# Kernel optimization log

Hardware: AMD Instinct MI355X
Metric: run time of the kernel (lower is better)

## Reference

```python
import jax, jax.numpy as jnp
import numpy as np

BN_EPS = 1e-5
N_SH, N_SS, N_HH, D = 1195, 390, 805, 64


def _gcn(x, edge_index, W, b, n_nodes, mean):
    # per-edge message = Linear(x_j); lin(x)[src] == lin(x[src])
    h = x @ W + b                                   # [N, out]
    msg = h[edge_index[0]]                          # gather sources -> [E, out]
    agg = jax.ops.segment_sum(msg, edge_index[1], num_segments=n_nodes)
    if mean:
        cnt = jax.ops.segment_sum(jnp.ones((edge_index.shape[1],), x.dtype),
                                  edge_index[1], num_segments=n_nodes)
        agg = agg / jnp.maximum(cnt, 1.0)[:, None]
    return jnp.tanh(agg)


def _bn(x, gamma, beta):
    # BatchNorm1d in training mode: biased batch statistics
    m = jnp.mean(x, axis=0)
    v = jnp.var(x, axis=0)
    return (x - m) * jax.lax.rsqrt(v + BN_EPS) * gamma + beta


def setup_inputs() -> dict:
    key = jax.random.key(0)
    ks = jax.random.split(key, 40)
    f32 = jnp.float32

    def lin(k, din, dout):
        k1, k2 = jax.random.split(k)
        s = 1.0 / np.sqrt(din)
        W = jax.random.uniform(k1, (din, dout), f32, -s, s)
        b = jax.random.uniform(k2, (dout,), f32, -s, s)
        return W, b

    inp = {}
    inp["x_SH"] = jnp.arange(N_SH, dtype=jnp.int64 if jax.config.jax_enable_x64 else jnp.int32)
    inp["edge_index_SH"] = jax.random.randint(ks[0], (2, 1_000_000), 0, N_SH)
    inp["x_SS"] = jnp.arange(N_SS)
    inp["edge_index_SS"] = jax.random.randint(ks[1], (2, 200_000), 0, N_SS)
    inp["x_HH"] = jnp.arange(N_HH)
    inp["edge_index_HH"] = jax.random.randint(ks[2], (2, 200_000), 0, N_HH)
    inp["prescription"] = jax.random.uniform(ks[3], (20000, N_SS), f32)
    inp["kgOneHot"] = jax.random.uniform(ks[4], (N_HH, 27), f32)

    inp["emb"] = jax.random.normal(ks[5], (N_SH, D), f32)
    inp["w_sh1"], inp["b_sh1"] = lin(ks[6], D, D)
    inp["w_sh2"], inp["b_sh2"] = lin(ks[7], D, D)
    inp["w_mlp1"], inp["b_mlp1"] = lin(ks[8], D, 256)
    inp["g_bn1"] = jnp.ones((256,), f32); inp["be_bn1"] = jnp.zeros((256,), f32)
    inp["w_sh1h"], inp["b_sh1h"] = lin(ks[9], D, D)
    inp["w_sh2h"], inp["b_sh2h"] = lin(ks[10], D, D)
    inp["w_mlp1h"], inp["b_mlp1h"] = lin(ks[11], D, 256)
    inp["g_bn1h"] = jnp.ones((256,), f32); inp["be_bn1h"] = jnp.zeros((256,), f32)
    inp["w_ss"], inp["b_ss"] = lin(ks[12], D, 256)
    inp["w_hh"], inp["b_hh"] = lin(ks[13], D + 27, 256)
    inp["w_mlp"], inp["b_mlp"] = lin(ks[14], 256, 256)
    inp["g_si"] = jnp.ones((256,), f32); inp["be_si"] = jnp.zeros((256,), f32)
    return inp


def reference(x_SH, edge_index_SH, x_SS, edge_index_SS, x_HH, edge_index_HH,
              prescription, kgOneHot, emb,
              w_sh1, b_sh1, w_sh2, b_sh2, w_mlp1, b_mlp1, g_bn1, be_bn1,
              w_sh1h, b_sh1h, w_sh2h, b_sh2h, w_mlp1h, b_mlp1h, g_bn1h, be_bn1h,
              w_ss, b_ss, w_hh, b_hh, w_mlp, b_mlp, g_si, be_si):
    # symptom branch on SH graph (mean aggregation)
    x1 = emb[x_SH]                                           # [1195, 64]
    x2 = _gcn(x1, edge_index_SH, w_sh1, b_sh1, N_SH, mean=True)
    x6 = _gcn(x2, edge_index_SH, w_sh2, b_sh2, N_SH, mean=True)
    x9 = (x1 + x2 + x6) / 3.0
    x9 = jnp.tanh(_bn(x9 @ w_mlp1 + b_mlp1, g_bn1, be_bn1))  # [1195, 256]

    # herb branch on SH graph
    x22 = _gcn(x1, edge_index_SH, w_sh1h, b_sh1h, N_SH, mean=True)
    x66 = _gcn(x22, edge_index_SH, w_sh2h, b_sh2h, N_SH, mean=True)
    x99 = (x1 + x22 + x66) / 3.0
    x99 = jnp.tanh(_bn(x99 @ w_mlp1h + b_mlp1h, g_bn1h, be_bn1h))

    # SS graph (add aggregation)
    x_ss1 = _gcn(emb[x_SS], edge_index_SS, w_ss, b_ss, N_SS, mean=False)  # [390, 256]

    # HH graph with KG one-hot features appended
    x_hh0 = jnp.concatenate([emb[x_HH], kgOneHot], axis=-1)  # [805, 91]
    x_hh1 = _gcn(x_hh0, edge_index_HH, w_hh, b_hh, N_HH, mean=False)      # [805, 256]

    es = x9[:N_SS] + x_ss1                                   # [390, 256]
    eh = x99[N_SS:] + x_hh1                                  # [805, 256]

    e_synd = prescription @ es                               # [B, 256]
    pre_sum = jnp.sum(prescription, axis=1, keepdims=True)
    e = e_synd / pre_sum
    e = jax.nn.relu(_bn(e @ w_mlp + b_mlp, g_si, be_si))
    return e @ eh.T                                          # [B, 805]
```

## Files before the change

### kernel.cpp

```cpp
#include <hip/hip_runtime.h>
#include <cstddef>
#include <cstdint>

#define N_SH 1195
#define N_SS 390
#define N_HH 805
#define DIM  64

typedef __bf16 bf16_t;
typedef bf16_t bf16x4v __attribute__((ext_vector_type(4)));
typedef bf16_t bf16x8v __attribute__((ext_vector_type(8)));
typedef float f32x4 __attribute__((ext_vector_type(4)));

__device__ inline ushort f2bf(float f) {
    union { float f; uint32_t u; } c; c.f = f;
    uint32_t u = c.u;
    u += 0x7FFFu + ((u >> 16) & 1u);
    return (ushort)(u >> 16);
}

__device__ inline void xcd_swizzle(int gx, int gy, int& bx, int& by) {
    int nwg = gx * gy;
    int lin = by * gx + bx;
    int q = nwg >> 3, r = nwg & 7;
    int xcd = lin & 7, idx = lin >> 3;
    int nt = (xcd < r ? xcd * (q + 1) : r * (q + 1) + (xcd - r) * q) + idx;
    by = nt / gx; bx = nt % gx;
}

__global__ void build_adj3_kernel(
    const int* __restrict__ e1, int E1, int hs1, uint32_t* __restrict__ T1,
    const int* __restrict__ e2, int E2, int hs2, uint32_t* __restrict__ T2,
    const int* __restrict__ e3, int E3, int hs3, uint32_t* __restrict__ T3)
{
    int i = blockIdx.x * blockDim.x + threadIdx.x;
    if (i < E1) {
        int src = e1[i], dst = e1[E1 + i];
        atomicAdd(&T1[(size_t)dst * hs1 + (src >> 2)], 1u << ((src & 3) * 8));
    } else if (i < E1 + E2) {
        int j = i - E1;
        int src = e2[j], dst = e2[E2 + j];
        atomicAdd(&T2[(size_t)dst * hs2 + (src >> 2)], 1u << ((src & 3) * 8));
    } else if (i < E1 + E2 + E3) {
        int j = i - E1 - E2;
        int src = e3[j], dst = e3[E3 + j];
        atomicAdd(&T3[(size_t)dst * hs3 + (src >> 2)], 1u << ((src & 3) * 8));
    }
}

__device__ inline void unpack_one(const uint32_t* __restrict__ T, int R, int C,
                                  int hs, ushort* __restrict__ out, int Cp, int i) {
    int r = i / Cp, c = i % Cp;
    float v = 0.f;
    if (r < R && c < C) {
        uint32_t w = T[(size_t)r * hs + (c >> 2)];
        v = (float)((w >> ((c & 3) * 8)) & 0xFFu);
    }
    out[i] = f2bf(v);
}

__global__ void mega_prep_kernel(
    const uint32_t* __restrict__ T1, int hs1, ushort* __restrict__ o1, int n1, int Cp1,
    const uint32_t* __restrict__ T2, int hs2, ushort* __restrict__ o2, int n2, int Cp2,
    const uint32_t* __restrict__ T3, int hs3, ushort* __restrict__ o3, int n3, int Cp3,
    float* __restrict__ cntInv,
    const float* __restrict__ w_sh1, const float* __restrict__ w_sh1h,
    const float* __restrict__ b_sh1, const float* __restrict__ b_sh1h,
    const float* __restrict__ w_sh2, const float* __restrict__ w_sh2h,
    const float* __restrict__ b_sh2, const float* __restrict__ b_sh2h,
    const float* __restrict__ w_mlp1, const float* __restrict__ w_mlp1h,
    const float* __restrict__ b_mlp1, const float* __restrict__ b_mlp1h,
    float* __restrict__ W1cat, float* __restrict__ b1cat,
    float* __restrict__ W2bd,  float* __restrict__ b2cat,
    float* __restrict__ WMbd,  float* __restrict__ bMcat,
    const float* __restrict__ emb, const float* __restrict__ kg,
    float* __restrict__ xhh0)
{
    int i = blockIdx.x * blockDim.x + threadIdx.x;
    if (i < n1) { unpack_one(T1, N_SH, N_SH, hs1, o1, Cp1, i); return; }
    i -= n1;
    if (i < n2) { unpack_one(T2, N_SS, N_SS, hs2, o2, Cp2, i); return; }
    i -= n2;
    if (i < n3) { unpack_one(T3, N_HH, N_HH, hs3, o3, Cp3, i); return; }
    i -= n3;
    if (i < N_SH * 64) {
        int row = i >> 6, lane = i & 63;
        const uint32_t* p = T1 + (size_t)row * hs1;
        uint32_t s = 0;
        for (int c = lane; c < hs1; c += 64) {
            uint32_t w0 = p[c];
            s += (w0 & 0xFFu) + ((w0 >> 8) & 0xFFu) + ((w0 >> 16) & 0xFFu) + (w0 >> 24);
        }
        for (int off = 32; off > 0; off >>= 1) s += __shfl_down(s, off);
        if (lane == 0) cntInv[row] = 1.0f / fmaxf((float)s, 1.0f);
        return;
    }
    i -= N_SH * 64;
    if (i < 64 * 128) {
        int k = i >> 7, j = i & 127;
        W1cat[i] = (j < 64) ? w_sh1[k * 64 + j] : w_sh1h[k * 64 + (j - 64)];
        return;
    }
    i -= 64 * 128;
    if (i < 128) { b1cat[i] = (i < 64) ? b_sh1[i] : b_sh1h[i - 64]; return; }
    i -= 128;
    if (i < 128 * 128) {
        int k = i >> 7, j = i & 127;
        float v = 0.f;
        if (k < 64 && j < 64) v = w_sh2[k * 64 + j];
        else if (k >= 64 && j >= 64) v = w_sh2h[(k - 64) * 64 + (j - 64)];
        W2bd[i] = v;
        return;
    }
    i -= 128 * 128;
    if (i < 128) { b2cat[i] = (i < 64) ? b_sh2[i] : b_sh2h[i - 64]; return; }
    i -= 128;
    if (i < 128 * 512) {
        int k = i >> 9, j = i & 511;
        float v = 0.f;
        if (j < 256) { if (k < 64) v = w_mlp1[k * 256 + j]; }
        else         { if (k >= 64) v = w_mlp1h[(k - 64) * 256 + (j - 256)]; }
        WMbd[i] = v;
        return;
    }
    i -= 128 * 512;
    if (i < 512) { bMcat[i] = (i < 256) ? b_mlp1[i] : b_mlp1h[i - 256]; return; }
    i -= 512;
    if (i < N_HH * 91) {
        int r = i / 91, c = i % 91;
        xhh0[i] = (c < DIM) ? emb[r * DIM + c] : kg[r * 27 + (c - DIM)];
    }
}

#define BM 64
#define BN 64
#define BK 16

__global__ __launch_bounds__(256) void gemm_kernel(
    const float* __restrict__ A, const float* __restrict__ A2, int ldaA, int ldaA2,
    const float* __restrict__ B,
    const float* __restrict__ bias,
    float* __restrict__ C, ushort* __restrict__ outT, int ldt,
    int M, int N, int K, float* __restrict__ statsOut, int statsStride,
    const float* __restrict__ bnStats, const float* __restrict__ bnG,
    const float* __restrict__ bnBe, int bnM)
{
    __shared__ float As[BK][BM + 4];
    __shared__ float Bs[BK][BN];
    __shared__ float cs[128];
    __shared__ float sA[256], tA[256];
    const int tid  = threadIdx.x;
    const int row0 = blockIdx.y * BM;
    const int col0 = blockIdx.x * BN;
    const int tr  = (tid >> 4) << 2;
    const int tc  = (tid & 15) << 2;
    const int lar = tid >> 2;
    const int lac = (tid & 3) << 2;
    const int lbr = tid >> 4;
    const int lbc = (tid & 15) << 2;

    if (bnStats) {
        float invM = 1.0f / (float)bnM;
        float mean = bnStats[tid] * invM;
        float var  = fmaxf(bnStats[512 + tid] * invM - mean * mean, 0.f);
        float scv  = bnG[tid] * rsqrtf(var + 1e-5f);
        sA[tid] = scv;
        tA[tid] = bnBe[tid] - mean * scv;
        __syncthreads();
    }

    float acc[4][4] = {{0.f}};

    for (int k0 = 0; k0 < K; k0 += BK) {
        const int gr = row0 + lar;
        #pragma unroll
        for (int i = 0; i < 4; ++i) {
            int gk = k0 + lac + i;
            float v = 0.f;
            if (gr < M && gk < K) {
                v = A[(size_t)gr * ldaA + gk];
                if (bnStats) v = tanhf(v * sA[gk] + tA[gk]);
                if (A2) v += A2[(size_t)gr * ldaA2 + gk];
            }
            As[lac + i][lar] = v;
        }
        const int gk = k0 + lbr;
        const float* Bp = B + (size_t)gk * N + col0 + lbc;
        #pragma unroll
        for (int i = 0; i < 4; ++i) {
            int gc = col0 + lbc + i;
            Bs[lbr][lbc + i] = (gk < K && gc < N) ? Bp[i] : 0.f;
        }
        __syncthreads();
        #pragma unroll
        for (int kk = 0; kk < BK; ++kk) {
            float4 a = *reinterpret_cast<const float4*>(&As[kk][tr]);
            float4 b = *reinterpret_cast<const float4*>(&Bs[kk][tc]);
            acc[0][0] += a.x * b.x; acc[0][1] += a.x * b.y; acc[0][2] += a.x * b.z; acc[0][3] += a.x * b.w;
            acc[1][0] += a.y * b.x; acc[1][1] += a.y * b.y; acc[1][2] += a.y * b.z; acc[1][3] += a.y * b.w;
            acc[2][0] += a.z * b.x; acc[2][1] += a.z * b.y; acc[2][2] += a.z * b.z; acc[2][3] += a.z * b.w;
            acc[3][0] += a.w * b.x; acc[3][1] += a.w * b.y; acc[3][2] += a.w * b.z; acc[3][3] += a.w * b.w;
        }
        __syncthreads();
    }

    float ls[4] = {0.f, 0.f, 0.f, 0.f}, lq[4] = {0.f, 0.f, 0.f, 0.f};
    #pragma unroll
    for (int i = 0; i < 4; ++i) {
        int gr = row0 + tr + i;
        if (gr >= M) continue;
        #pragma unroll
        for (int j = 0; j < 4; ++j) {
            int gc = col0 + tc + j;
            if (gc >= N) continue;
            float v = acc[i][j];
            if (bias) v += bias[gc];
            if (outT) outT[(size_t)gc * ldt + gr] = f2bf(v);
            else      C[(size_t)gr * N + gc] = v;
            ls[j] += v; lq[j] += v * v;
        }
    }

    if (statsOut) {
        if (tid < 128) cs[tid] = 0.f;
        __syncthreads();
        #pragma unroll
        for (int j = 0; j < 4; ++j) {
            atomicAdd(&cs[tc + j], ls[j]);
            atomicAdd(&cs[64 + tc + j], lq[j]);
        }
        __syncthreads();
        if (tid < 64) {
            atomicAdd(&statsOut[col0 + tid], cs[tid]);
            atomicAdd(&statsOut[statsStride + col0 + tid], cs[64 + tid]);
        }
    }
}

#define LDT 40
#define OLW 132

__device__ inline void loadP8(const float* __restrict__ rowp, int c0, bool rv,
                              float* a, float& s) {
    if (rv && c0 + 8 <= N_SS) {
        float2 x0 = *reinterpret_cast<const float2*>(rowp + c0);
        float2 x1 = *reinterpret_cast<const float2*>(rowp + c0 + 2);
        float2 x2 = *reinterpret_cast<const float2*>(rowp + c0 + 4);
        float2 x3 = *reinterpret_cast<const float2*>(rowp + c0 + 6);
        a[0] = x0.x; a[1] = x0.y; a[2] = x1.x; a[3] = x1.y;
        a[4] = x2.x; a[5] = x2.y; a[6] = x3.x; a[7] = x3.y;
    } else {
        #pragma unroll
        for (int i = 0; i < 8; ++i) a[i] = (rv && (c0 + i) < N_SS) ? rowp[c0 + i] : 0.f;
    }
    #pragma unroll
    for (int i = 0; i < 8; ++i) s += a[i];
}

__global__ __launch_bounds__(256) void mfma_c1_kernel(
    const float* __restrict__ Pm, const ushort* __restrict__ Dt,
    int M, const float* __restrict__ bias,
    float* __restrict__ outF, float* __restrict__ statsOut)
{
    __shared__ __align__(16) uint8_t smemRaw[128 * LDT * 2 * 2];
    ushort* As = (ushort*)smemRaw;
    ushort* Bs = (ushort*)(smemRaw + 128 * LDT * 2);
    float*  oLds = (float*)smemRaw;
    __shared__ float sums[128];
    __shared__ float cs[256];
    const int tid  = threadIdx.x;
    int bx = blockIdx.x, by = blockIdx.y;
    xcd_swizzle(gridDim.x, gridDim.y, bx, by);
    const int row0 = by * 128;
    const int col0 = bx * 128;
    const int wid  = tid >> 6, lane = tid & 63;
    const int wr = wid >> 1, wc = wid & 1;
    const int l15 = lane & 15, lg = lane >> 4;
    const int kg = lg * 4;
    const int sr = tid >> 2;
    const int sc = (tid & 3) * 8;

    const float* pA0 = Pm + (size_t)(row0 + sr)      * N_SS;
    const float* pA1 = Pm + (size_t)(row0 + sr + 64) * N_SS;
    const bool rv0 = (row0 + sr)      < M;
    const bool rv1 = (row0 + sr + 64) < M;
    const ushort* pB0 = Dt + (size_t)(col0 + sr)      * 416 + sc;
    const ushort* pB1 = Dt + (size_t)(col0 + sr + 64) * 416 + sc;

    float a0[8], a1[8];
    float s0 = 0.f, s1 = 0.f;
    loadP8(pA0, sc, rv0, a0, s0);
    loadP8(pA1, sc, rv1, a1, s1);
    uint4 b0 = *reinterpret_cast<const uint4*>(pB0);
    uint4 b1 = *reinterpret_cast<const uint4*>(pB1);

    f32x4 acc[4][4];
    #pragma unroll
    for (int m = 0; m < 4; ++m)
        #pragma unroll
        for (int n = 0; n < 4; ++n) acc[m][n] = (f32x4)0.f;

    for (int k0 = 0; k0 < 416; k0 += 32) {
        {
            bf16_t h[8];
            #pragma unroll
            for (int i = 0; i < 8; ++i) h[i] = (bf16_t)a0[i];
            *reinterpret_cast<uint4*>(&As[sr * LDT + sc]) = *reinterpret_cast<const uint4*>(h);
            #pragma unroll
            for (int i = 0; i < 8; ++i) h[i] = (bf16_t)a1[i];
            *reinterpret_cast<uint4*>(&As[(sr + 64) * LDT + sc]) = *reinterpret_cast<const uint4*>(h);
        }
        *reinterpret_cast<uint4*>(&Bs[sr * LDT + sc])        = b0;
        *reinterpret_cast<uint4*>(&Bs[(sr + 64) * LDT + sc]) = b1;
        __syncthreads();
        if (k0 + 32 < 416) {
            loadP8(pA0, k0 + 32 + sc, rv0, a0, s0);
            loadP8(pA1, k0 + 32 + sc, rv1, a1, s1);
            b0 = *reinterpret_cast<const uint4*>(pB0 + k0 + 32);
            b1 = *reinterpret_cast<const uint4*>(pB1 + k0 + 32);
        }

        bf16x8v af[4], bfr[4];
        #pragma unroll
        for (int m = 0; m < 4; ++m) {
            int ar = wr * 64 + m * 16 + l15;
            bf16x4v lo = *reinterpret_cast<const bf16x4v*>(&As[ar * LDT + kg]);
            bf16x4v hi = *reinterpret_cast<const bf16x4v*>(&As[ar * LDT + kg + 16]);
            af[m] = __builtin_shufflevector(lo, hi, 0, 1, 2, 3, 4, 5, 6, 7);
        }
        #pragma unroll
        for (int n = 0; n < 4; ++n) {
            int br = wc * 64 + n * 16 + l15;
            bf16x4v lo = *reinterpret_cast<const bf16x4v*>(&Bs[br * LDT + kg]);
            bf16x4v hi = *reinterpret_cast<const bf16x4v*>(&Bs[br * LDT + kg + 16]);
            bfr[n] = __builtin_shufflevector(lo, hi, 0, 1, 2, 3, 4, 5, 6, 7);
        }
        #pragma unroll
        for (int m = 0; m < 4; ++m)
            #pragma unroll
            for (int n = 0; n < 4; ++n)
                acc[m][n] = __builtin_amdgcn_mfma_f32_16x16x32_bf16(af[m], bfr[n], acc[m][n], 0, 0, 0);
        __syncthreads();
    }

    if (tid < 128) sums[tid] = 0.f;
    if (tid < 256) cs[tid] = 0.f;
    __syncthreads();
    atomicAdd(&sums[sr], s0);
    atomicAdd(&sums[sr + 64], s1);
    __syncthreads();

    float ls[4] = {0.f, 0.f, 0.f, 0.f}, lq[4] = {0.f, 0.f, 0.f, 0.f};
    #pragma unroll
    for (int m = 0; m < 4; ++m) {
        int lr_base = wr * 64 + m * 16 + kg;
        #pragma unroll
        for (int j = 0; j < 4; ++j) {
            int lr = lr_base + j;
            int grow = row0 + lr;
            float t = sums[lr];
            float inv = (t != 0.f) ? 1.0f / t : 0.f;
            #pragma unroll
            for (int n = 0; n < 4; ++n) {
                int gcol = col0 + wc * 64 + n * 16 + l15;
                float v = acc[m][n][j] * inv + bias[gcol];
                acc[m][n][j] = v;
                if (grow < M) { ls[n] += v; lq[n] += v * v; }
            }
        }
    }

    #pragma unroll
    for (int n = 0; n < 4; ++n) {
        int lc = wc * 64 + n * 16 + l15;
        atomicAdd(&cs[lc], ls[n]);
        atomicAdd(&cs[128 + lc], lq[n]);
    }
    __syncthreads();
    if (tid < 128) {
        atomicAdd(&statsOut[col0 + tid], cs[tid]);
        atomicAdd(&statsOut[256 + col0 + tid], cs[128 + tid]);
    }

    for (int m = 0; m < 4; ++m) {
        __syncthreads();
        #pragma unroll
        for (int n = 0; n < 4; ++n)
            #pragma unroll
            for (int j = 0; j < 4; ++j)
                oLds[(wr * 16 + kg + j) * OLW + wc * 64 + n * 16 + l15] = acc[m][n][j];
        __syncthreads();
        #pragma unroll
        for (int rr = 0; rr < 8; ++rr) {
            int lrow = wid * 8 + rr;
            int band = lrow >> 4;
            int r16  = lrow & 15;
            int grow = row0 + band * 64 + m * 16 + r16;
            if (grow < M) {
                float v0 = oLds[lrow * OLW + lane];
                float v1 = oLds[lrow * OLW + 64 + lane];
                outF[(size_t)grow * 256 + col0 + lane]      = v0;
                outF[(size_t)grow * 256 + col0 + 64 + lane] = v1;
            }
        }
    }
}

__global__ __launch_bounds__(256) void mfma_c3_kernel(
    const float* __restrict__ Abuf, const ushort* __restrict__ Bt,
    int M, int Nw,
    const float* __restrict__ stats, const float* __restrict__ g,
    const float* __restrict__ be,
    float* __restrict__ outF, int ldo)
{
    __shared__ __align__(16) uint8_t smemRaw[128 * LDT * 2 * 2];
    ushort* As = (ushort*)smemRaw;
    ushort* Bs = (ushort*)(smemRaw + 128 * LDT * 2);
    float*  oLds = (float*)smemRaw;
    __shared__ float sscale[256], sshift[256];
    const int tid  = threadIdx.x;
    int bx = blockIdx.x, by = blockIdx.y;
    xcd_swizzle(gridDim.x, gridDim.y, bx, by);
    const int row0 = by * 128;
    const int col0 = bx * 128;
    const int wid  = tid >> 6, lane = tid & 63;
    const int wr = wid >> 1, wc = wid & 1;
    const int l15 = lane & 15, lg = lane >> 4;
    const int kg = lg * 4;
    const int sr = tid >> 2;
    const int sc = (tid & 3) * 8;

    if (tid < 256) {
        float invM = 1.0f / (float)M;
        float mean = stats[tid] * invM;
        float var  = fmaxf(stats[256 + tid] * invM - mean * mean, 0.f);
        float scv  = g[tid] * rsqrtf(var + 1e-5f);
        sscale[tid] = scv;
        sshift[tid] = be[tid] - mean * scv;
    }
    __syncthreads();

    const float*  pA0 = Abuf + (size_t)(row0 + sr)      * 256 + sc;
    const float*  pA1 = Abuf + (size_t)(row0 + sr + 64) * 256 + sc;
    const ushort* pB0 = Bt + (size_t)(col0 + sr)        * 256 + sc;
    const ushort* pB1 = Bt + (size_t)(col0 + sr + 64)   * 256 + sc;

    float4 a00 = *reinterpret_cast<const float4*>(pA0);
    float4 a01 = *reinterpret_cast<const float4*>(pA0 + 4);
    float4 a10 = *reinterpret_cast<const float4*>(pA1);
    float4 a11 = *reinterpret_cast<const float4*>(pA1 + 4);
    uint4  b0  = *reinterpret_cast<const uint4*>(pB0);
    uint4  b1  = *reinterpret_cast<const uint4*>(pB1);

    f32x4 acc[4][4];
    #pragma unroll
    for (int m = 0; m < 4; ++m)
        #pragma unroll
        for (int n = 0; n < 4; ++n) acc[m][n] = (f32x4)0.f;

    for (int k0 = 0; k0 < 256; k0 += 32) {
        float s8[8], t8[8];
        #pragma unroll
        for (int i = 0; i < 8; ++i) { s8[i] = sscale[k0 + sc + i]; t8[i] = sshift[k0 + sc + i]; }
        {
            bf16_t h[8];
            h[0] = (bf16_t)fmaxf(a00.x * s8[0] + t8[0], 0.f);
            h[1] = (bf16_t)fmaxf(a00.y * s8[1] + t8[1], 0.f);
            h[2] = (bf16_t)fmaxf(a00.z * s8[2] + t8[2], 0.f);
            h[3] = (bf16_t)fmaxf(a00.w * s8[3] + t8[3], 0.f);
            h[4] = (bf16_t)fmaxf(a01.x * s8[4] + t8[4], 0.f);
            h[5] = (bf16_t)fmaxf(a01.y * s8[5] + t8[5], 0.f);
            h[6] = (bf16_t)fmaxf(a01.z * s8[6] + t8[6], 0.f);
            h[7] = (bf16_t)fmaxf(a01.w * s8[7] + t8[7], 0.f);
            *reinterpret_cast<uint4*>(&As[sr * LDT + sc]) = *reinterpret_cast<const uint4*>(h);
            h[0] = (bf16_t)fmaxf(a10.x * s8[0] + t8[0], 0.f);
            h[1] = (bf16_t)fmaxf(a10.y * s8[1] + t8[1], 0.f);
            h[2] = (bf16_t)fmaxf(a10.z * s8[2] + t8[2], 0.f);
            h[3] = (bf16_t)fmaxf(a10.w * s8[3] + t8[3], 0.f);
            h[4] = (bf16_t)fmaxf(a11.x * s8[4] + t8[4], 0.f);
            h[5] = (bf16_t)fmaxf(a11.y * s8[5] + t8[5], 0.f);
            h[6] = (bf16_t)fmaxf(a11.z * s8[6] + t8[6], 0.f);
            h[7] = (bf16_t)fmaxf(a11.w * s8[7] + t8[7], 0.f);
            *reinterpret_cast<uint4*>(&As[(sr + 64) * LDT + sc]) = *reinterpret_cast<const uint4*>(h);
        }
        *reinterpret_cast<uint4*>(&Bs[sr * LDT + sc])        = b0;
        *reinterpret_cast<uint4*>(&Bs[(sr + 64) * LDT + sc]) = b1;
        __syncthreads();
        if (k0 + 32 < 256) {
            a00 = *reinterpret_cast<const float4*>(pA0 + k0 + 32);
            a01 = *reinterpret_cast<const float4*>(pA0 + k0 + 36);
            a10 = *reinterpret_cast<const float4*>(pA1 + k0 + 32);
            a11 = *reinterpret_cast<const float4*>(pA1 + k0 + 36);
            b0  = *reinterpret_cast<const uint4*>(pB0 + k0 + 32);
            b1  = *reinterpret_cast<const uint4*>(pB1 + k0 + 32);
        }

        bf16x8v af[4], bfr[4];
        #pragma unroll
        for (int m = 0; m < 4; ++m) {
            int ar = wr * 64 + m * 16 + l15;
            bf16x4v lo = *reinterpret_cast<const bf16x4v*>(&As[ar * LDT + kg]);
            bf16x4v hi = *reinterpret_cast<const bf16x4v*>(&As[ar * LDT + kg + 16]);
            af[m] = __builtin_shufflevector(lo, hi, 0, 1, 2, 3, 4, 5, 6, 7);
        }
        #pragma unroll
        for (int n = 0; n < 4; ++n) {
            int br = wc * 64 + n * 16 + l15;
            bf16x4v lo = *reinterpret_cast<const bf16x4v*>(&Bs[br * LDT + kg]);
            bf16x4v hi = *reinterpret_cast<const bf16x4v*>(&Bs[br * LDT + kg + 16]);
            bfr[n] = __builtin_shufflevector(lo, hi, 0, 1, 2, 3, 4, 5, 6, 7);
        }
        #pragma unroll
        for (int m = 0; m < 4; ++m)
            #pragma unroll
            for (int n = 0; n < 4; ++n)
                acc[m][n] = __builtin_amdgcn_mfma_f32_16x16x32_bf16(af[m], bfr[n], acc[m][n], 0, 0, 0);
        __syncthreads();
    }

    for (int m = 0; m < 4; ++m) {
        __syncthreads();
        #pragma unroll
        for (int n = 0; n < 4; ++n)
            #pragma unroll
            for (int j = 0; j < 4; ++j)
                oLds[(wr * 16 + kg + j) * OLW + wc * 64 + n * 16 + l15] = acc[m][n][j];
        __syncthreads();
        #pragma unroll
        for (int rr = 0; rr < 8; ++rr) {
            int lrow = wid * 8 + rr;
            int band = lrow >> 4;
            int r16  = lrow & 15;
            int grow = row0 + band * 64 + m * 16 + r16;
            if (grow < M) {
                float v0 = oLds[lrow * OLW + lane];
                float v1 = oLds[lrow * OLW + 64 + lane];
                int gc0 = col0 + lane;
                int gc1 = col0 + 64 + lane;
                if (gc0 < Nw) outF[(size_t)grow * ldo + gc0] = v0;
                if (gc1 < Nw) outF[(size_t)grow * ldo + gc1] = v1;
            }
        }
    }
}

__global__ __launch_bounds__(256) void mfma_splitk_kernel(
    const ushort* __restrict__ A, const ushort* __restrict__ Bt,
    int M, int K, int lda, int kChunk, int Ntot,
    float* __restrict__ part)
{
    __shared__ __align__(16) ushort As[128 * LDT];
    __shared__ __align__(16) ushort Bs[128 * LDT];
    const int tid  = threadIdx.x;
    const int row0 = blockIdx.y * 128;
    const int col0 = blockIdx.x * 128;
    const int wid  = tid >> 6, lane = tid & 63;
    const int wr = wid >> 1, wc = wid & 1;
    const int l15 = lane & 15, lg = lane >> 4;
    const int kg = lg * 4;
    const int sr = tid >> 2;
    const int sc = (tid & 3) * 8;

    const int k0s = blockIdx.z * kChunk;
    const int k0e = (k0s + kChunk < K) ? k0s + kChunk : K;

    const ushort* pA0 = A  + (size_t)(row0 + sr)      * lda + sc;
    const ushort* pA1 = A  + (size_t)(row0 + sr + 64) * lda + sc;
    const ushort* pB0 = Bt + (size_t)(col0 + sr)      * lda + sc;
    const ushort* pB1 = Bt + (size_t)(col0 + sr + 64) * lda + sc;

    uint4 ra0 = *reinterpret_cast<const uint4*>(pA0 + k0s);
    uint4 ra1 = *reinterpret_cast<const uint4*>(pA1 + k0s);
    uint4 rb0 = *reinterpret_cast<const uint4*>(pB0 + k0s);
    uint4 rb1 = *reinterpret_cast<const uint4*>(pB1 + k0s);

    f32x4 acc[4][4];
    #pragma unroll
    for (int m = 0; m < 4; ++m)
        #pragma unroll
        for (int n = 0; n < 4; ++n) acc[m][n] = (f32x4)0.f;

    for (int k0 = k0s; k0 < k0e; k0 += 32) {
        *reinterpret_cast<uint4*>(&As[sr * LDT + sc])        = ra0;
        *reinterpret_cast<uint4*>(&As[(sr + 64) * LDT + sc]) = ra1;
        *reinterpret_cast<uint4*>(&Bs[sr * LDT + sc])        = rb0;
        *reinterpret_cast<uint4*>(&Bs[(sr + 64) * LDT + sc]) = rb1;
        __syncthreads();
        if (k0 + 32 < k0e) {
            ra0 = *reinterpret_cast<const uint4*>(pA0 + k0 + 32);
            ra1 = *reinterpret_cast<const uint4*>(pA1 + k0 + 32);
            rb0 = *reinterpret_cast<const uint4*>(pB0 + k0 + 32);
            rb1 = *reinterpret_cast<const uint4*>(pB1 + k0 + 32);
        }

        bf16x8v af[4], bfr[4];
        #pragma unroll
        for (int m = 0; m < 4; ++m) {
            int ar = wr * 64 + m * 16 + l15;
            bf16x4v lo = *reinterpret_cast<const bf16x4v*>(&As[ar * LDT + kg]);
            bf16x4v hi = *reinterpret_cast<const bf16x4v*>(&As[ar * LDT + kg + 16]);
            af[m] = __builtin_shufflevector(lo, hi, 0, 1, 2, 3, 4, 5, 6, 7);
        }
        #pragma unroll
        for (int n = 0; n < 4; ++n) {
            int br = wc * 64 + n * 16 + l15;
            bf16x4v lo = *reinterpret_cast<const bf16x4v*>(&Bs[br * LDT + kg]);
            bf16x4v hi = *reinterpret_cast<const bf16x4v*>(&Bs[br * LDT + kg + 16]);
            bfr[n] = __builtin_shufflevector(lo, hi, 0, 1, 2, 3, 4, 5, 6, 7);
        }
        #pragma unroll
        for (int m = 0; m < 4; ++m)
            #pragma unroll
            for (int n = 0; n < 4; ++n)
                acc[m][n] = __builtin_amdgcn_mfma_f32_16x16x32_bf16(af[m], bfr[n], acc[m][n], 0, 0, 0);
        __syncthreads();
    }

    float* pslab = part + (size_t)blockIdx.z * M * Ntot;
    #pragma unroll
    for (int m = 0; m < 4; ++m) {
        int grow_base = row0 + wr * 64 + m * 16 + kg;
        #pragma unroll
        for (int j = 0; j < 4; ++j) {
            int grow = grow_base + j;
            if (grow >= M) continue;
            #pragma unroll
            for (int n = 0; n < 4; ++n) {
                int gcol = col0 + wc * 64 + n * 16 + l15;
                pslab[(size_t)grow * Ntot + gcol] = acc[m][n][j];
            }
        }
    }
}

__global__ void reduce_tanh_kernel(const float* __restrict__ part, int S, int M, int N,
                                   const float* __restrict__ rs,
                                   const float* __restrict__ emb,
                                   const float* __restrict__ prev,
                                   float* __restrict__ out) {
    int i = blockIdx.x * blockDim.x + threadIdx.x;
    if (i >= M * N) return;
    int r = i / N, j = i - r * N;
    float s = 0.f;
    for (int z = 0; z < S; ++z) s += part[(size_t)z * M * N + i];
    if (rs) s *= rs[r];
    float t = tanhf(s);
    if (emb) out[i] = (emb[r * 64 + (j & 63)] + prev[i] + t) * (1.0f / 3.0f);
    else     out[i] = t;
}

__global__ void make_ehb_bn_kernel(const float* __restrict__ tmpBN,
                                   const float* __restrict__ stats,
                                   const float* __restrict__ g, const float* __restrict__ be,
                                   const float* __restrict__ hh1,
                                   ushort* __restrict__ out, int Rp) {
    int i = blockIdx.x * blockDim.x + threadIdx.x;
    if (i >= Rp * 256) return;
    int r = i >> 8, c = i & 255;
    float v = 0.f;
    if (r < N_HH) {
        float invM = 1.0f / (float)N_SH;
        int j = 256 + c;
        float mean = stats[j] * invM;
        float var  = fmaxf(stats[512 + j] * invM - mean * mean, 0.f);
        float x = tmpBN[(size_t)(N_SS + r) * 512 + j];
        float y = tanhf((x - mean) * rsqrtf(var + 1e-5f) * g[c] + be[c]);
        v = y + hh1[(size_t)r * 256 + c];
    }
    out[i] = f2bf(v);
}

extern "C" void kernel_launch(void* const* d_in, const int* in_sizes, int n_in,
                              void* d_out, int out_size, void* d_ws, size_t ws_size,
                              hipStream_t stream) {
    const int*   eiSH = (const int*)d_in[1];
    const int*   eiSS = (const int*)d_in[3];
    const int*   eiHH = (const int*)d_in[5];
    const float* P    = (const float*)d_in[6];
    const float* kg   = (const float*)d_in[7];
    const float* emb  = (const float*)d_in[8];
    const float* w_sh1  = (const float*)d_in[9];   const float* b_sh1  = (const float*)d_in[10];
    const float* w_sh2  = (const float*)d_in[11];  const float* b_sh2  = (const float*)d_in[12];
    const float* w_mlp1 = (const float*)d_in[13];  const float* b_mlp1 = (const float*)d_in[14];
    const float* g_bn1  = (const float*)d_in[15];  const float* be_bn1 = (const float*)d_in[16];
    const float* w_sh1h = (const float*)d_in[17];  const float* b_sh1h = (const float*)d_in[18];
    const float* w_sh2h = (const float*)d_in[19];  const float* b_sh2h = (const float*)d_in[20];
    const float* w_mlp1h= (const float*)d_in[21];  const float* b_mlp1h= (const float*)d_in[22];
    const float* g_bn1h = (const float*)d_in[23];  const float* be_bn1h= (const float*)d_in[24];
    const float* w_ss   = (const float*)d_in[25];  const float* b_ss   = (const float*)d_in[26];
    const float* w_hh   = (const float*)d_in[27];  const float* b_hh   = (const float*)d_in[28];
    const float* w_mlp  = (const float*)d_in[29];  const float* b_mlp  = (const float*)d_in[30];
    const float* g_si   = (const float*)d_in[31];  const float* be_si  = (const float*)d_in[32];
    float* out = (float*)d_out;

    const int E_SH = in_sizes[1] / 2;
    const int E_SS = in_sizes[3] / 2;
    const int E_HH = in_sizes[5] / 2;
    const int B    = in_sizes[6] / N_SS;
    const int Mp   = ((B + 127) / 128) * 128;
    const int KP1  = 416;
    const int NP3  = 896;
    const int KSH  = 1216;
    const int KHH  = 832;
    const int HS_SH = (N_SH + 3) / 4;
    const int HS_SS = (N_SS + 3) / 4;
    const int HS_HH = (N_HH + 3) / 4;

    float* w = (float*)d_ws;
    size_t off = 0;
    auto alloc = [&](size_t n) { float* p = w + off; off += (n + 3) & ~(size_t)3; return p; };

    float* cntInv   = alloc(N_SH);
    float* statsCat = alloc(1024);
    float* statsC2  = alloc(512);
    ushort* HT      = (ushort*)alloc((size_t)128 * KSH / 2);
    ushort* HSST    = (ushort*)alloc((size_t)256 * KP1 / 2);
    ushort* HHHT    = (ushort*)alloc((size_t)256 * KHH / 2);
    ushort* eswT    = (ushort*)alloc((size_t)256 * KP1 / 2);
    float* zeroEnd  = w + off;
    float* W1cat   = alloc(64 * 128);
    float* b1cat   = alloc(128);
    float* W2bd    = alloc(128 * 128);
    float* b2cat   = alloc(128);
    float* WMbd    = alloc(128 * 512);
    float* bMcat   = alloc(512);
    ushort* adjb   = (ushort*)alloc((size_t)1280 * KSH / 2);
    ushort* adjSSb = (ushort*)alloc((size_t)512 * KP1 / 2);
    ushort* adjHHb = (ushort*)alloc((size_t)896 * KHH / 2);
    float* x2cat   = alloc((size_t)N_SH * 128);
    float* x9a2    = alloc((size_t)N_SH * 128);
    float* tmpBN   = alloc((size_t)N_SH * 512);
    float* ss1     = alloc((size_t)N_SS * 256);
    float* hh1     = alloc((size_t)N_HH * 256);
    float* xhh0    = alloc((size_t)N_HH * 91);
    ushort* eh_b   = (ushort*)alloc((size_t)NP3 * 256 / 2);
    float* regionA = alloc((size_t)Mp * 256);
    uint32_t* uSH  = (uint32_t*)regionA;
    uint32_t* uSS  = uSH + (size_t)N_SH * HS_SH;
    uint32_t* uHH  = uSS + (size_t)N_SS * HS_SS;
    size_t packed_words = (size_t)N_SH * HS_SH + (size_t)N_SS * HS_SS + (size_t)N_HH * HS_HH;
    float*  bufM   = regionA;
    float* regionB = alloc((size_t)Mp * 256);
    float*  partials = regionB;
    (void)ws_size; (void)n_in; (void)out_size;

    auto gemmT = [&](const float* Am, const float* A2m, int lda1, int lda2,
                     const float* Bm, const float* bias,
                     ushort* oT, int ldt, int M, int N, int K,
                     const float* bnS, const float* bnG, const float* bnB, int bnM) {
        dim3 g((N + BN - 1) / BN, (M + BM - 1) / BM);
        gemm_kernel<<<g, 256, 0, stream>>>(Am, A2m, lda1, lda2, Bm, bias,
                                           nullptr, oT, ldt, M, N, K, nullptr, 0,
                                           bnS, bnG, bnB, bnM);
    };
    auto gemmF = [&](const float* Am, const float* Bm, const float* bias,
                     float* C, int M, int N, int K, float* st, int sstride) {
        dim3 g((N + BN - 1) / BN, (M + BM - 1) / BM);
        gemm_kernel<<<g, 256, 0, stream>>>(Am, nullptr, K, 0, Bm, bias,
                                           C, nullptr, 0, M, N, K, st, sstride,
                                           nullptr, nullptr, nullptr, 0);
    };
    auto splitk = [&](const ushort* Am, const ushort* Bm, int M, int Mtiles, int K, int lda,
                      int Ntot, int S, const float* rs, const float* embA, const float* prev,
                      float* outp) {
        dim3 g(Ntot / 128, Mtiles, S);
        mfma_splitk_kernel<<<g, 256, 0, stream>>>(Am, Bm, M, K, lda, 128, Ntot, partials);
        reduce_tanh_kernel<<<(M * Ntot + 255) / 256, 256, 0, stream>>>(
            partials, S, M, Ntot, rs, embA, prev, outp);
    };

    hipMemsetAsync(uSH, 0, packed_words * sizeof(uint32_t), stream);
    hipMemsetAsync(statsCat, 0, (size_t)((char*)zeroEnd - (char*)statsCat), stream);

    {
        int Etot = E_SH + E_SS + E_HH;
        build_adj3_kernel<<<(Etot + 255) / 256, 256, 0, stream>>>(
            eiSH, E_SH, HS_SH, uSH, eiSS, E_SS, HS_SS, uSS, eiHH, E_HH, HS_HH, uHH);
    }
    {
        int n1 = 1280 * KSH, n2 = 512 * KP1, n3 = 896 * KHH;
        int tot = n1 + n2 + n3 + N_SH * 64 + 90880 + N_HH * 91;
        mega_prep_kernel<<<(tot + 255) / 256, 256, 0, stream>>>(
            uSH, HS_SH, adjb, n1, KSH, uSS, HS_SS, adjSSb, n2, KP1,
            uHH, HS_HH, adjHHb, n3, KHH, cntInv,
            w_sh1, w_sh1h, b_sh1, b_sh1h, w_sh2, w_sh2h, b_sh2, b_sh2h,
            w_mlp1, w_mlp1h, b_mlp1, b_mlp1h,
            W1cat, b1cat, W2bd, b2cat, WMbd, bMcat,
            emb, kg, xhh0);
    }

    gemmT(emb, nullptr, 64, 0, W1cat, b1cat, HT, KSH, N_SH, 128, 64,
          nullptr, nullptr, nullptr, 0);
    splitk(adjb, HT, N_SH, 10, KSH, KSH, 128, 10, cntInv, nullptr, nullptr, x2cat);
    gemmT(x2cat, nullptr, 128, 0, W2bd, b2cat, HT, KSH, N_SH, 128, 128,
          nullptr, nullptr, nullptr, 0);
    splitk(adjb, HT, N_SH, 10, KSH, KSH, 128, 10, cntInv, emb, x2cat, x9a2);
    gemmF(x9a2, WMbd, bMcat, tmpBN, N_SH, 512, 128, statsCat, 512);

    gemmT(emb, nullptr, 64, 0, w_ss, b_ss, HSST, KP1, N_SS, 256, 64,
          nullptr, nullptr, nullptr, 0);
    splitk(adjSSb, HSST, N_SS, 4, KP1, KP1, 256, 4, nullptr, nullptr, nullptr, ss1);

    gemmT(xhh0, nullptr, 91, 0, w_hh, b_hh, HHHT, KHH, N_HH, 256, 91,
          nullptr, nullptr, nullptr, 0);
    splitk(adjHHb, HHHT, N_HH, 7, KHH, KHH, 256, 7, nullptr, nullptr, nullptr, hh1);

    make_ehb_bn_kernel<<<(NP3 * 256 + 255) / 256, 256, 0, stream>>>(
        tmpBN, statsCat, g_bn1h, be_bn1h, hh1, eh_b, NP3);

    gemmT(tmpBN, ss1, 512, 256, w_mlp, nullptr, eswT, KP1, N_SS, 256, 256,
          statsCat, g_bn1, be_bn1, N_SH);
    {
        dim3 g(2, (B + 127) / 128);
        mfma_c1_kernel<<<g, 256, 0, stream>>>(P, eswT, B, b_mlp, bufM, statsC2);
    }
    {
        dim3 g(NP3 / 128, (B + 127) / 128);
        mfma_c3_kernel<<<g, 256, 0, stream>>>(bufM, eh_b, B, N_HH, statsC2, g_si, be_si, out, N_HH);
    }
}
```

Baseline: 318.4 us.

## Batch SS and HH GCN branches into shared launches and fold memset into prep

The separate SS and HH projection GEMMs and split-K aggregations are merged into combined kernels that pick their branch by blockIdx.z, and one reduce kernel handles both. The hipMemsetAsync that zeroed the stats and transposed buffers is dropped, and that zeroing moves into the mega prep kernel. The aim is fewer kernel launches and better GPU fill for the two small independent branches. It adds branching in the kernels and depends on the zeroed region layout being correct (HT through the side buffers, statsCat).

```diff
diff --git a/kernel.cpp b/kernel.cpp
--- a/kernel.cpp
+++ b/kernel.cpp
@@ -74,7 +74,9 @@
     float* __restrict__ W2bd,  float* __restrict__ b2cat,
     float* __restrict__ WMbd,  float* __restrict__ bMcat,
     const float* __restrict__ emb, const float* __restrict__ kg,
-    float* __restrict__ xhh0)
+    float* __restrict__ xhh0,
+    float* __restrict__ zeroF, int nZeroF,
+    ushort* __restrict__ zeroH, int nZeroH)
 {
     int i = blockIdx.x * blockDim.x + threadIdx.x;
     if (i < n1) { unpack_one(T1, N_SH, N_SH, hs1, o1, Cp1, i); return; }
@@ -129,29 +131,31 @@
     if (i < N_HH * 91) {
         int r = i / 91, c = i % 91;
         xhh0[i] = (c < DIM) ? emb[r * DIM + c] : kg[r * 27 + (c - DIM)];
-    }
+        return;
+    }
+    i -= N_HH * 91;
+    if (i < nZeroF) { zeroF[i] = 0.f; return; }
+    i -= nZeroF;
+    if (i < nZeroH) { zeroH[i] = 0; }
 }
 
 #define BM 64
 #define BN 64
 #define BK 16
 
-__global__ __launch_bounds__(256) void gemm_kernel(
+__device__ __forceinline__ void gemm_body(
     const float* __restrict__ A, const float* __restrict__ A2, int ldaA, int ldaA2,
-    const float* __restrict__ B,
-    const float* __restrict__ bias,
+    const float* __restrict__ B, const float* __restrict__ bias,
     float* __restrict__ C, ushort* __restrict__ outT, int ldt,
     int M, int N, int K, float* __restrict__ statsOut, int statsStride,
     const float* __restrict__ bnStats, const float* __restrict__ bnG,
-    const float* __restrict__ bnBe, int bnM)
+    const float* __restrict__ bnBe, int bnM,
+    int bx, int by, int tid,
+    float* __restrict__ AsBuf, float* __restrict__ BsBuf,
+    float* __restrict__ cs, float* __restrict__ sA, float* __restrict__ tA)
 {
-    __shared__ float As[BK][BM + 4];
-    __shared__ float Bs[BK][BN];
-    __shared__ float cs[128];
-    __shared__ float sA[256], tA[256];
-    const int tid  = threadIdx.x;
-    const int row0 = blockIdx.y * BM;
-    const int col0 = blockIdx.x * BN;
+    const int row0 = by * BM;
+    const int col0 = bx * BN;
     const int tr  = (tid >> 4) << 2;
     const int tc  = (tid & 15) << 2;
     const int lar = tid >> 2;
@@ -182,20 +186,20 @@
                 if (bnStats) v = tanhf(v * sA[gk] + tA[gk]);
                 if (A2) v += A2[(size_t)gr * ldaA2 + gk];
             }
-            As[lac + i][lar] = v;
+            AsBuf[(lac + i) * (BM + 4) + lar] = v;
         }
         const int gk = k0 + lbr;
         const float* Bp = B + (size_t)gk * N + col0 + lbc;
         #pragma unroll
         for (int i = 0; i < 4; ++i) {
             int gc = col0 + lbc + i;
-            Bs[lbr][lbc + i] = (gk < K && gc < N) ? Bp[i] : 0.f;
+            BsBuf[lbr * BN + lbc + i] = (gk < K && gc < N) ? Bp[i] : 0.f;
         }
         __syncthreads();
         #pragma unroll
         for (int kk = 0; kk < BK; ++kk) {
-            float4 a = *reinterpret_cast<const float4*>(&As[kk][tr]);
-            float4 b = *reinterpret_cast<const float4*>(&Bs[kk][tc]);
+            float4 a = *reinterpret_cast<const float4*>(&AsBuf[kk * (BM + 4) + tr]);
+            float4 b = *reinterpret_cast<const float4*>(&BsBuf[kk * BN + tc]);
             acc[0][0] += a.x * b.x; acc[0][1] += a.x * b.y; acc[0][2] += a.x * b.z; acc[0][3] += a.x * b.w;
             acc[1][0] += a.y * b.x; acc[1][1] += a.y * b.y; acc[1][2] += a.y * b.z; acc[1][3] += a.y * b.w;
             acc[2][0] += a.z * b.x; acc[2][1] += a.z * b.y; acc[2][2] += a.z * b.z; acc[2][3] += a.z * b.w;
@@ -237,8 +241,198 @@
     }
 }
 
+__global__ __launch_bounds__(256) void gemm_kernel(
+    const float* __restrict__ A, const float* __restrict__ A2, int ldaA, int ldaA2,
+    const float* __restrict__ B, const float* __restrict__ bias,
+    float* __restrict__ C, ushort* __restrict__ outT, int ldt,
+    int M, int N, int K, float* __restrict__ statsOut, int statsStride,
+    const float* __restrict__ bnStats, const float* __restrict__ bnG,
+    const float* __restrict__ bnBe, int bnM)
+{
+    __shared__ float As[BK * (BM + 4)];
+    __shared__ float Bs[BK * BN];
+    __shared__ float cs[128];
+    __shared__ float sA[256], tA[256];
+    gemm_body(A, A2, ldaA, ldaA2, B, bias, C, outT, ldt, M, N, K,
+              statsOut, statsStride, bnStats, bnG, bnBe, bnM,
+              blockIdx.x, blockIdx.y, threadIdx.x, As, Bs, cs, sA, tA);
+}
+
+__global__ __launch_bounds__(256) void gemm_side_kernel(
+    const float* __restrict__ emb, const float* __restrict__ w_ss,
+    const float* __restrict__ b_ss, ushort* __restrict__ HSST,
+    const float* __restrict__ xhh0, const float* __restrict__ w_hh,
+    const float* __restrict__ b_hh, ushort* __restrict__ HHHT,
+    int KP1v, int KHHv)
+{
+    __shared__ float As[BK * (BM + 4)];
+    __shared__ float Bs[BK * BN];
+    __shared__ float cs[128];
+    __shared__ float sA[256], tA[256];
+    if (blockIdx.z == 0) {
+        if (blockIdx.y >= 7) return;
+        gemm_body(emb, nullptr, 64, 0, w_ss, b_ss, nullptr, HSST, KP1v,
+                  N_SS, 256, 64, nullptr, 0, nullptr, nullptr, nullptr, 0,
+                  blockIdx.x, blockIdx.y, threadIdx.x, As, Bs, cs, sA, tA);
+    } else {
+        gemm_body(xhh0, nullptr, 91, 0, w_hh, b_hh, nullptr, HHHT, KHHv,
+                  N_HH, 256, 91, nullptr, 0, nullptr, nullptr, nullptr, 0,
+                  blockIdx.x, blockIdx.y, threadIdx.x, As, Bs, cs, sA, tA);
+    }
+}
+
 #define LDT 40
 #define OLW 132
+
+__device__ __forceinline__ void splitk_body(
+    const ushort* __restrict__ A, const ushort* __restrict__ Bt,
+    int M, int K, int lda, int kChunk, int Ntot,
+    float* __restrict__ part, int bx, int by, int bz, int tid,
+    ushort* __restrict__ As, ushort* __restrict__ Bs)
+{
+    const int row0 = by * 128;
+    const int col0 = bx * 128;
+    const int wid  = tid >> 6, lane = tid & 63;
+    const int wr = wid >> 1, wc = wid & 1;
+    const int l15 = lane & 15, lg = lane >> 4;
+    const int kg = lg * 4;
+    const int sr = tid >> 2;
+    const int sc = (tid & 3) * 8;
+
+    const int k0s = bz * kChunk;
+    const int k0e = (k0s + kChunk < K) ? k0s + kChunk : K;
+
+    const ushort* pA0 = A  + (size_t)(row0 + sr)      * lda + sc;
+    const ushort* pA1 = A  + (size_t)(row0 + sr + 64) * lda + sc;
+    const ushort* pB0 = Bt + (size_t)(col0 + sr)      * lda + sc;
+    const ushort* pB1 = Bt + (size_t)(col0 + sr + 64) * lda + sc;
+
+    uint4 ra0 = *reinterpret_cast<const uint4*>(pA0 + k0s);
+    uint4 ra1 = *reinterpret_cast<const uint4*>(pA1 + k0s);
+    uint4 rb0 = *reinterpret_cast<const uint4*>(pB0 + k0s);
+    uint4 rb1 = *reinterpret_cast<const uint4*>(pB1 + k0s);
+
+    f32x4 acc[4][4];
+    #pragma unroll
+    for (int m = 0; m < 4; ++m)
+        #pragma unroll
+        for (int n = 0; n < 4; ++n) acc[m][n] = (f32x4)0.f;
+
+    for (int k0 = k0s; k0 < k0e; k0 += 32) {
+        *reinterpret_cast<uint4*>(&As[sr * LDT + sc])        = ra0;
+        *reinterpret_cast<uint4*>(&As[(sr + 64) * LDT + sc]) = ra1;
+        *reinterpret_cast<uint4*>(&Bs[sr * LDT + sc])        = rb0;
+        *reinterpret_cast<uint4*>(&Bs[(sr + 64) * LDT + sc]) = rb1;
+        __syncthreads();
+        if (k0 + 32 < k0e) {
+            ra0 = *reinterpret_cast<const uint4*>(pA0 + k0 + 32);
+            ra1 = *reinterpret_cast<const uint4*>(pA1 + k0 + 32);
+            rb0 = *reinterpret_cast<const uint4*>(pB0 + k0 + 32);
+            rb1 = *reinterpret_cast<const uint4*>(pB1 + k0 + 32);
+        }
+
+        bf16x8v af[4], bfr[4];
+        #pragma unroll
+        for (int m = 0; m < 4; ++m) {
+            int ar = wr * 64 + m * 16 + l15;
+            bf16x4v lo = *reinterpret_cast<const bf16x4v*>(&As[ar * LDT + kg]);
+            bf16x4v hi = *reinterpret_cast<const bf16x4v*>(&As[ar * LDT + kg + 16]);
+            af[m] = __builtin_shufflevector(lo, hi, 0, 1, 2, 3, 4, 5, 6, 7);
+        }
+        #pragma unroll
+        for (int n = 0; n < 4; ++n) {
+            int br = wc * 64 + n * 16 + l15;
+            bf16x4v lo = *reinterpret_cast<const bf16x4v*>(&Bs[br * LDT + kg]);
+            bf16x4v hi = *reinterpret_cast<const bf16x4v*>(&Bs[br * LDT + kg + 16]);
+            bfr[n] = __builtin_shufflevector(lo, hi, 0, 1, 2, 3, 4, 5, 6, 7);
+        }
+        #pragma unroll
+        for (int m = 0; m < 4; ++m)
+            #pragma unroll
+            for (int n = 0; n < 4; ++n)
+                acc[m][n] = __builtin_amdgcn_mfma_f32_16x16x32_bf16(af[m], bfr[n], acc[m][n], 0, 0, 0);
+        __syncthreads();
+    }
+
+    float* pslab = part + (size_t)bz * M * Ntot;
+    #pragma unroll
+    for (int m = 0; m < 4; ++m) {
+        int grow_base = row0 + wr * 64 + m * 16 + kg;
+        #pragma unroll
+        for (int j = 0; j < 4; ++j) {
+            int grow = grow_base + j;
+            if (grow >= M) continue;
+            #pragma unroll
+            for (int n = 0; n < 4; ++n) {
+                int gcol = col0 + wc * 64 + n * 16 + l15;
+                pslab[(size_t)grow * Ntot + gcol] = acc[m][n][j];
+            }
+        }
+    }
+}
+
+__global__ __launch_bounds__(256) void mfma_splitk_kernel(
+    const ushort* __restrict__ A, const ushort* __restrict__ Bt,
+    int M, int K, int lda, int kChunk, int Ntot, float* __restrict__ part)
+{
+    __shared__ __align__(16) ushort As[128 * LDT];
+    __shared__ __align__(16) ushort Bs[128 * LDT];
+    splitk_body(A, Bt, M, K, lda, kChunk, Ntot, part,
+                blockIdx.x, blockIdx.y, blockIdx.z, threadIdx.x, As, Bs);
+}
+
+__global__ __launch_bounds__(256) void mfma_splitk_side_kernel(
+    const ushort* __restrict__ adjSS, const ushort* __restrict__ HSST, int KP1v,
+    float* __restrict__ pSS,
+    const ushort* __restrict__ adjHH, const ushort* __restrict__ HHHT, int KHHv,
+    float* __restrict__ pHH)
+{
+    __shared__ __align__(16) ushort As[128 * LDT];
+    __shared__ __align__(16) ushort Bs[128 * LDT];
+    if (blockIdx.z < 4) {
+        if (blockIdx.y >= 4) return;
+        splitk_body(adjSS, HSST, N_SS, KP1v, KP1v, 128, 256, pSS,
+                    blockIdx.x, blockIdx.y, blockIdx.z, threadIdx.x, As, Bs);
+    } else {
+        splitk_body(adjHH, HHHT, N_HH, KHHv, KHHv, 128, 256, pHH,
+                    blockIdx.x, blockIdx.y, blockIdx.z - 4, threadIdx.x, As, Bs);
+    }
+}
+
+__global__ void reduce_tanh_kernel(const float* __restrict__ part, int S, int M, int N,
+                                   const float* __restrict__ rs,
+                                   const float* __restrict__ emb,
+                                   const float* __restrict__ prev,
+                                   float* __restrict__ out) {
+    int i = blockIdx.x * blockDim.x + threadIdx.x;
+    if (i >= M * N) return;
+    int r = i / N, j = i - r * N;
+    float s = 0.f;
+    for (int z = 0; z < S; ++z) s += part[(size_t)z * M * N + i];
+    if (rs) s *= rs[r];
+    float t = tanhf(s);
+    if (emb) out[i] = (emb[r * 64 + (j & 63)] + prev[i] + t) * (1.0f / 3.0f);
+    else     out[i] = t;
+}
+
+__global__ void reduce_side_kernel(const float* __restrict__ pSS, float* __restrict__ ss1,
+                                   const float* __restrict__ pHH, float* __restrict__ hh1) {
+    int i = blockIdx.x * blockDim.x + threadIdx.x;
+    const int nSS = N_SS * 256;
+    const int nHH = N_HH * 256;
+    if (i < nSS) {
+        float s = 0.f;
+        for (int z = 0; z < 4; ++z) s += pSS[(size_t)z * nSS + i];
+        ss1[i] = tanhf(s);
+        return;
+    }
+    i -= nSS;
+    if (i < nHH) {
+        float s = 0.f;
+        for (int z = 0; z < 7; ++z) s += pHH[(size_t)z * nHH + i];
+        hh1[i] = tanhf(s);
+    }
+}
 
 __device__ inline void loadP8(const float* __restrict__ rowp, int c0, bool rv,
                               float* a, float& s) {
@@ -544,111 +738,6 @@
     }
 }
 
-__global__ __launch_bounds__(256) void mfma_splitk_kernel(
-    const ushort* __restrict__ A, const ushort* __restrict__ Bt,
-    int M, int K, int lda, int kChunk, int Ntot,
-    float* __restrict__ part)
-{
-    __shared__ __align__(16) ushort As[128 * LDT];
-    __shared__ __align__(16) ushort Bs[128 * LDT];
-    const int tid  = threadIdx.x;
-    const int row0 = blockIdx.y * 128;
-    const int col0 = blockIdx.x * 128;
-    const int wid  = tid >> 6, lane = tid & 63;
-    const int wr = wid >> 1, wc = wid & 1;
-    const int l15 = lane & 15, lg = lane >> 4;
-    const int kg = lg * 4;
-    const int sr = tid >> 2;
-    const int sc = (tid & 3) * 8;
-
-    const int k0s = blockIdx.z * kChunk;
-    const int k0e = (k0s + kChunk < K) ? k0s + kChunk : K;
-
-    const ushort* pA0 = A  + (size_t)(row0 + sr)      * lda + sc;
-    const ushort* pA1 = A  + (size_t)(row0 + sr + 64) * lda + sc;
-    const ushort* pB0 = Bt + (size_t)(col0 + sr)      * lda + sc;
-    const ushort* pB1 = Bt + (size_t)(col0 + sr + 64) * lda + sc;
-
-    uint4 ra0 = *reinterpret_cast<const uint4*>(pA0 + k0s);
-    uint4 ra1 = *reinterpret_cast<const uint4*>(pA1 + k0s);
-    uint4 rb0 = *reinterpret_cast<const uint4*>(pB0 + k0s);
-    uint4 rb1 = *reinterpret_cast<const uint4*>(pB1 + k0s);
-
-    f32x4 acc[4][4];
-    #pragma unroll
-    for (int m = 0; m < 4; ++m)
-        #pragma unroll
-        for (int n = 0; n < 4; ++n) acc[m][n] = (f32x4)0.f;
-
-    for (int k0 = k0s; k0 < k0e; k0 += 32) {
-        *reinterpret_cast<uint4*>(&As[sr * LDT + sc])        = ra0;
-        *reinterpret_cast<uint4*>(&As[(sr + 64) * LDT + sc]) = ra1;
-        *reinterpret_cast<uint4*>(&Bs[sr * LDT + sc])        = rb0;
-        *reinterpret_cast<uint4*>(&Bs[(sr + 64) * LDT + sc]) = rb1;
-        __syncthreads();
-        if (k0 + 32 < k0e) {
-            ra0 = *reinterpret_cast<const uint4*>(pA0 + k0 + 32);
-            ra1 = *reinterpret_cast<const uint4*>(pA1 + k0 + 32);
-            rb0 = *reinterpret_cast<const uint4*>(pB0 + k0 + 32);
-            rb1 = *reinterpret_cast<const uint4*>(pB1 + k0 + 32);
-        }
-
-        bf16x8v af[4], bfr[4];
-        #pragma unroll
-        for (int m = 0; m < 4; ++m) {
-            int ar = wr * 64 + m * 16 + l15;
-            bf16x4v lo = *reinterpret_cast<const bf16x4v*>(&As[ar * LDT + kg]);
-            bf16x4v hi = *reinterpret_cast<const bf16x4v*>(&As[ar * LDT + kg + 16]);
-            af[m] = __builtin_shufflevector(lo, hi, 0, 1, 2, 3, 4, 5, 6, 7);
-        }
-        #pragma unroll
-        for (int n = 0; n < 4; ++n) {
-            int br = wc * 64 + n * 16 + l15;
-            bf16x4v lo = *reinterpret_cast<const bf16x4v*>(&Bs[br * LDT + kg]);
-            bf16x4v hi = *reinterpret_cast<const bf16x4v*>(&Bs[br * LDT + kg + 16]);
-            bfr[n] = __builtin_shufflevector(lo, hi, 0, 1, 2, 3, 4, 5, 6, 7);
-        }
-        #pragma unroll
-        for (int m = 0; m < 4; ++m)
-            #pragma unroll
-            for (int n = 0; n < 4; ++n)
-                acc[m][n] = __builtin_amdgcn_mfma_f32_16x16x32_bf16(af[m], bfr[n], acc[m][n], 0, 0, 0);
-        __syncthreads();
-    }
-
-    float* pslab = part + (size_t)blockIdx.z * M * Ntot;
-    #pragma unroll
-    for (int m = 0; m < 4; ++m) {
-        int grow_base = row0 + wr * 64 + m * 16 + kg;
-        #pragma unroll
-        for (int j = 0; j < 4; ++j) {
-            int grow = grow_base + j;
-            if (grow >= M) continue;
-            #pragma unroll
-            for (int n = 0; n < 4; ++n) {
-                int gcol = col0 + wc * 64 + n * 16 + l15;
-                pslab[(size_t)grow * Ntot + gcol] = acc[m][n][j];
-            }
-        }
-    }
-}
-
-__global__ void reduce_tanh_kernel(const float* __restrict__ part, int S, int M, int N,
-                                   const float* __restrict__ rs,
-                                   const float* __restrict__ emb,
-                                   const float* __restrict__ prev,
-                                   float* __restrict__ out) {
-    int i = blockIdx.x * blockDim.x + threadIdx.x;
-    if (i >= M * N) return;
-    int r = i / N, j = i - r * N;
-    float s = 0.f;
-    for (int z = 0; z < S; ++z) s += part[(size_t)z * M * N + i];
-    if (rs) s *= rs[r];
-    float t = tanhf(s);
-    if (emb) out[i] = (emb[r * 64 + (j & 63)] + prev[i] + t) * (1.0f / 3.0f);
-    else     out[i] = t;
-}
-
 __global__ void make_ehb_bn_kernel(const float* __restrict__ tmpBN,
                                    const float* __restrict__ stats,
                                    const float* __restrict__ g, const float* __restrict__ be,
@@ -717,7 +806,6 @@
     ushort* HSST    = (ushort*)alloc((size_t)256 * KP1 / 2);
     ushort* HHHT    = (ushort*)alloc((size_t)256 * KHH / 2);
     ushort* eswT    = (ushort*)alloc((size_t)256 * KP1 / 2);
-    float* zeroEnd  = w + off;
     float* W1cat   = alloc(64 * 128);
     float* b1cat   = alloc(128);
     float* W2bd    = alloc(128 * 128);
@@ -742,7 +830,12 @@
     float*  bufM   = regionA;
     float* regionB = alloc((size_t)Mp * 256);
     float*  partials = regionB;
+    float*  pSS = regionB;
+    float*  pHH = regionB + (size_t)4 * N_SS * 256;
     (void)ws_size; (void)n_in; (void)out_size;
+
+    const int nZeroF = 1536;
+    const int nZeroH = 128 * KSH + 256 * KP1 + 256 * KHH + 256 * KP1;
 
     auto gemmT = [&](const float* Am, const float* A2m, int lda1, int lda2,
                      const float* Bm, const float* bias,
@@ -770,7 +863,6 @@
     };
 
     hipMemsetAsync(uSH, 0, packed_words * sizeof(uint32_t), stream);
-    hipMemsetAsync(statsCat, 0, (size_t)((char*)zeroEnd - (char*)statsCat), stream);
 
     {
         int Etot = E_SH + E_SS + E_HH;
@@ -779,14 +871,29 @@
     }
     {
         int n1 = 1280 * KSH, n2 = 512 * KP1, n3 = 896 * KHH;
-        int tot = n1 + n2 + n3 + N_SH * 64 + 90880 + N_HH * 91;
-        mega_prep_kernel<<<(tot + 255) / 256, 256, 0, stream>>>(
+        long long tot = (long long)n1 + n2 + n3 + N_SH * 64 + 90880 + N_HH * 91
+                        + nZeroF + nZeroH;
+        mega_prep_kernel<<<(unsigned)((tot + 255) / 256), 256, 0, stream>>>(
             uSH, HS_SH, adjb, n1, KSH, uSS, HS_SS, adjSSb, n2, KP1,
             uHH, HS_HH, adjHHb, n3, KHH, cntInv,
             w_sh1, w_sh1h, b_sh1, b_sh1h, w_sh2, w_sh2h, b_sh2, b_sh2h,
             w_mlp1, w_mlp1h, b_mlp1, b_mlp1h,
             W1cat, b1cat, W2bd, b2cat, WMbd, bMcat,
-            emb, kg, xhh0);
+            emb, kg, xhh0,
+            statsCat, nZeroF, HT, nZeroH);
+    }
+
+    {
+        dim3 g(4, 13, 2);
+        gemm_side_kernel<<<g, 256, 0, stream>>>(emb, w_ss, b_ss, HSST,
+                                                xhh0, w_hh, b_hh, HHHT, KP1, KHH);
+    }
+    {
+        dim3 g(2, 7, 11);
+        mfma_splitk_side_kernel<<<g, 256, 0, stream>>>(
+            adjSSb, HSST, KP1, pSS, adjHHb, HHHT, KHH, pHH);
+        int totE = N_SS * 256 + N_HH * 256;
+        reduce_side_kernel<<<(totE + 255) / 256, 256, 0, stream>>>(pSS, ss1, pHH, hh1);
     }
 
     gemmT(emb, nullptr, 64, 0, W1cat, b1cat, HT, KSH, N_SH, 128, 64,
@@ -797,14 +904,6 @@
     splitk(adjb, HT, N_SH, 10, KSH, KSH, 128, 10, cntInv, emb, x2cat, x9a2);
     gemmF(x9a2, WMbd, bMcat, tmpBN, N_SH, 512, 128, statsCat, 512);
 
-    gemmT(emb, nullptr, 64, 0, w_ss, b_ss, HSST, KP1, N_SS, 256, 64,
-          nullptr, nullptr, nullptr, 0);
-    splitk(adjSSb, HSST, N_SS, 4, KP1, KP1, 256, 4, nullptr, nullptr, nullptr, ss1);
-
-    gemmT(xhh0, nullptr, 91, 0, w_hh, b_hh, HHHT, KHH, N_HH, 256, 91,
-          nullptr, nullptr, nullptr, 0);
-    splitk(adjHHb, HHHT, N_HH, 7, KHH, KHH, 256, 7, nullptr, nullptr, nullptr, hh1);
-
     make_ehb_bn_kernel<<<(NP3 * 256 + 255) / 256, 256, 0, stream>>>(
         tmpBN, statsCat, g_bn1h, be_bn1h, hh1, eh_b, NP3);
 
```

Measured after the change: 295.6 us, median of 2. -7.1%, faster.
